# Performance work log

Measured on AMD Instinct MI355X. Metric: run time of the kernel, lower is better.

## Reference

```python
import jax, jax.numpy as jnp
import numpy as np

V, D, E, K = 8192, 128, 262144, 512

def _sqrtm_psd(A):
    # symmetric PSD matrix square root via eigendecomposition
    w, v = jnp.linalg.eigh(A)
    w = jnp.clip(w, 0.0)
    return (v * jnp.sqrt(w)) @ v.T


def setup_inputs() -> dict:
    key = jax.random.key(0)
    k1, k2, k3, k4 = jax.random.split(key, 4)
    inputs = jax.random.normal(k1, (V, D), dtype=jnp.float32) * 0.1
    # targets must be SPD (it is passed through sqrtm as a covariance)
    A = jax.random.normal(k2, (K, K), dtype=jnp.float32) / np.sqrt(K)
    targets = A @ A.T + 0.1 * jnp.eye(K, dtype=jnp.float32)
    edge_index = jax.random.randint(k3, (2, E), 0, V, dtype=jnp.int32)
    pmat = jax.random.normal(k4, (K, V), dtype=jnp.float32) / np.sqrt(V)
    return {"inputs": inputs, "targets": targets, "edge_index": edge_index, "pmat": pmat}


def reference(inputs, targets, edge_index, pmat):
    n = inputs.shape[0]
    i, j = edge_index[0], edge_index[1]
    # per-edge squared distance -> exp weight (vectorized gather-compute)
    d = jnp.sum((inputs[i] - inputs[j]) ** 2, axis=-1)  # [E]
    w = jnp.exp(-d)
    # W starts as identity (self loops give exp(0)=1, same as eye); symmetric scatter
    W = jnp.eye(n, dtype=inputs.dtype)
    W = W.at[i, j].set(w).at[j, i].set(w)
    deg = W.sum(axis=1)
    L = jnp.diag(deg) - W
    k = pmat.shape[0]
    L_adj = pmat @ L @ pmat.T + 1e-05 * jnp.eye(k, dtype=inputs.dtype)
    S1 = jnp.linalg.inv(L_adj)
    S0 = targets.astype(jnp.float32)
    S0_sqrt = _sqrtm_psd(S0)
    S_ = _sqrtm_psd(S0_sqrt @ S1 @ S0_sqrt)
    return jnp.trace(S1) + jnp.trace(S0) - 2.0 * jnp.trace(S_)
```

## Files before the change

### kernel.cpp

```cpp
#include <hip/hip_runtime.h>
#include <math.h>

#define VN 8192
#define DN 128
#define EN 262144
#define KD 512
#define KK (KD*KD)

#define S_SS_LADJ 0
#define S_INV_C1  1
#define S_SS_S0   2
#define S_INV_C0  3
#define S_QRT_C0  4
#define S_SS_G    5
#define S_INV_CG  6
#define S_QRT_CG  7
#define S_TR_X    8
#define S_TR_S0   9
#define S_TR_YG   10

typedef __attribute__((ext_vector_type(8))) __bf16 bf16x8;
typedef __attribute__((ext_vector_type(4))) float f32x4;

static __device__ __forceinline__ float waveReduceAdd(float v) {
#pragma unroll
  for (int o = 32; o; o >>= 1) v += __shfl_xor(v, o);
  return v;
}

static __device__ __forceinline__ ushort f2b(float f) {
  unsigned x = __float_as_uint(f);
  unsigned r = (x + 0x7fffu + ((x >> 16) & 1u)) >> 16;
  return (ushort)r;
}
static __device__ __forceinline__ float b2f(ushort u) {
  return __uint_as_float((unsigned)u << 16);
}


__global__ __launch_bounds__(256) void transpose_k(const float* __restrict__ in,
                                                   float* __restrict__ out) {
  __shared__ float s[32][33];
  int tx = threadIdx.x & 31, ty = threadIdx.x >> 5;
  int v0 = blockIdx.x * 32, k0 = blockIdx.y * 32;
  for (int r = ty; r < 32; r += 8) s[r][tx] = in[(size_t)(k0 + r) * VN + v0 + tx];
  __syncthreads();
  for (int r = ty; r < 32; r += 8) out[(size_t)(v0 + r) * KD + k0 + tx] = s[tx][r];
}

__global__ __launch_bounds__(256) void count_k(const float* __restrict__ x,
                                               const int* __restrict__ ei,
                                               int* __restrict__ ea, int* __restrict__ eb,
                                               float* __restrict__ ew,
                                               int* __restrict__ cnt,
                                               unsigned int* __restrict__ bitmap) {
  int e = (int)(((unsigned)blockIdx.x * 256u + threadIdx.x) >> 4);
  int lane = threadIdx.x & 63;
  int sl = lane & 15;
  if (e >= EN) return;
  int i = ei[e], j = ei[EN + e];
  int a = i < j ? i : j;
  int b = i < j ? j : i;
  int ok = 0;
  if (sl == 0) {
    if (i != j) {
      unsigned key = (unsigned)a * (unsigned)VN + (unsigned)b;
      unsigned m = 1u << (key & 31u);
      unsigned old = atomicOr(bitmap + (key >> 5), m);
      ok = (old & m) ? 0 : 1;
    }
  }
  ok = __shfl(ok, lane & 48);
  if (!ok) { if (sl == 0) ea[e] = -1; return; }
  const float4* xa = (const float4*)&x[(size_t)a * DN + sl * 8];
  const float4* xb = (const float4*)&x[(size_t)b * DN + sl * 8];
  float4 a0 = xa[0], a1 = xa[1], b0 = xb[0], b1 = xb[1];
  float d0 = a0.x - b0.x, d1 = a0.y - b0.y, d2 = a0.z - b0.z, d3 = a0.w - b0.w;
  float d4 = a1.x - b1.x, d5 = a1.y - b1.y, d6 = a1.z - b1.z, d7 = a1.w - b1.w;
  float s = d0*d0 + d1*d1 + d2*d2 + d3*d3 + d4*d4 + d5*d5 + d6*d6 + d7*d7;
#pragma unroll
  for (int o = 8; o; o >>= 1) s += __shfl_xor(s, o);
  if (sl == 0) {
    ea[e] = a; eb[e] = b; ew[e] = expf(-s);
    atomicAdd(cnt + a, 1);
    atomicAdd(cnt + b, 1);
  }
}

__global__ __launch_bounds__(1024) void scan_k(const int* __restrict__ cnt,
                                               int* __restrict__ rowptr,
                                               int* __restrict__ cursor) {
  __shared__ int sd[1024];
  __shared__ int carry;
  int tid = threadIdx.x;
  if (tid == 0) { carry = 0; rowptr[0] = 0; }
  __syncthreads();
  for (int c = 0; c < VN / 1024; ++c) {
    int v = c * 1024 + tid;
    int xv = cnt[v];
    sd[tid] = xv;
    __syncthreads();
    for (int off = 1; off < 1024; off <<= 1) {
      int t = (tid >= off) ? sd[tid - off] : 0;
      __syncthreads();
      sd[tid] += t;
      __syncthreads();
    }
    int incl = sd[tid];
    int base = carry;
    rowptr[v + 1] = base + incl;
    cursor[v] = base + incl - xv;
    __syncthreads();
    if (tid == 1023) carry = base + incl;
    __syncthreads();
  }
}

__global__ __launch_bounds__(256) void fill_k(const int* __restrict__ ea, const int* __restrict__ eb,
                                              const float* __restrict__ ew,
                                              int* __restrict__ cursor,
                                              int* __restrict__ adjj, float* __restrict__ adjw) {
  int e = blockIdx.x * 256 + threadIdx.x;
  if (e >= EN) return;
  int a = ea[e];
  if (a < 0) return;
  int b = eb[e];
  float w = ew[e];
  int p = atomicAdd(cursor + a, 1); adjj[p] = b; adjw[p] = w;
  int q = atomicAdd(cursor + b, 1); adjj[q] = a; adjw[q] = w;
}

__global__ __launch_bounds__(512) void buildB_k(const float* __restrict__ pmatT,
                                                const int* __restrict__ rowptr,
                                                const int* __restrict__ adjj,
                                                const float* __restrict__ adjw,
                                                float* __restrict__ Bout) {
  int v = blockIdx.x;
  int k = threadIdx.x;
  int s = rowptr[v], e = rowptr[v + 1];
  float a0 = 0.f, a1 = 0.f, a2 = 0.f, a3 = 0.f;
  float a4 = 0.f, a5 = 0.f, a6 = 0.f, a7 = 0.f, sw = 0.f;
  int p = s;
  for (; p + 8 <= e; p += 8) {
    int j0 = adjj[p],     j1 = adjj[p + 1], j2 = adjj[p + 2], j3 = adjj[p + 3];
    int j4 = adjj[p + 4], j5 = adjj[p + 5], j6 = adjj[p + 6], j7 = adjj[p + 7];
    float w0 = adjw[p],     w1 = adjw[p + 1], w2 = adjw[p + 2], w3 = adjw[p + 3];
    float w4 = adjw[p + 4], w5 = adjw[p + 5], w6 = adjw[p + 6], w7 = adjw[p + 7];
    a0 += w0 * pmatT[(size_t)j0 * KD + k];
    a1 += w1 * pmatT[(size_t)j1 * KD + k];
    a2 += w2 * pmatT[(size_t)j2 * KD + k];
    a3 += w3 * pmatT[(size_t)j3 * KD + k];
    a4 += w4 * pmatT[(size_t)j4 * KD + k];
    a5 += w5 * pmatT[(size_t)j5 * KD + k];
    a6 += w6 * pmatT[(size_t)j6 * KD + k];
    a7 += w7 * pmatT[(size_t)j7 * KD + k];
    sw += w0 + w1 + w2 + w3 + w4 + w5 + w6 + w7;
  }
  for (; p < e; ++p) {
    int jj = adjj[p];
    float w = adjw[p];
    a0 += w * pmatT[(size_t)jj * KD + k];
    sw += w;
  }
  Bout[(size_t)v * KD + k] = sw * pmatT[(size_t)v * KD + k]
                           - ((a0 + a1) + (a2 + a3) + (a4 + a5) + (a6 + a7));
}

__global__ __launch_bounds__(256) void gemm_big_k(const float* __restrict__ A,
                                                  const float* __restrict__ B,
                                                  float* __restrict__ C) {
  __shared__ __align__(16) float As[32][68];
  __shared__ __align__(16) float Bs[32][68];
  int tid = threadIdx.x;
  int tx = tid & 15, ty = tid >> 4;
  int n0 = blockIdx.x * 64, m0 = blockIdx.y * 64;
  int kbase = blockIdx.z * (VN / 8);
  float acc[4][4] = {};
  for (int kt = kbase; kt < kbase + VN / 8; kt += 32) {
#pragma unroll
    for (int u = 0; u < 2; ++u) {
      int li = tid * 2 + u;
      int r = li >> 3, c = (li & 7) * 4;
      float4 av = *(const float4*)&A[(size_t)(m0 + r) * VN + kt + c];
      As[c][r] = av.x; As[c + 1][r] = av.y; As[c + 2][r] = av.z; As[c + 3][r] = av.w;
      int rb = li >> 4, cb = (li & 15) * 4;
      *(float4*)&Bs[rb][cb] = *(const float4*)&B[(size_t)(kt + rb) * KD + n0 + cb];
    }
    __syncthreads();
#pragma unroll
    for (int k = 0; k < 32; ++k) {
      float4 av = *(const float4*)&As[k][ty * 4];
      float4 bv = *(const float4*)&Bs[k][tx * 4];
      float am[4] = {av.x, av.y, av.z, av.w};
      float bm[4] = {bv.x, bv.y, bv.z, bv.w};
#pragma unroll
      for (int mi = 0; mi < 4; ++mi)
#pragma unroll
        for (int ni = 0; ni < 4; ++ni) acc[mi][ni] += am[mi] * bm[ni];
    }
    __syncthreads();
  }
#pragma unroll
  for (int mi = 0; mi < 4; ++mi)
#pragma unroll
    for (int ni = 0; ni < 4; ++ni)
      atomicAdd(&C[(m0 + ty * 4 + mi) * KD + n0 + tx * 4 + ni], acc[mi][ni]);
}


static __device__ __forceinline__ void g32_body(const float* __restrict__ A,
                                                const float* __restrict__ B,
                                                const float* __restrict__ Dm,
                                                float* __restrict__ C,
                                                float alpha, float beta) {
  __shared__ __align__(16) float As[32][34];
  __shared__ __align__(16) float Bs[32][34];
  int tid = threadIdx.x;
  int tx = tid & 15, ty = tid >> 4;
  int n0 = blockIdx.x * 32, m0 = blockIdx.y * 32;
  float a00 = 0.f, a01 = 0.f, a10 = 0.f, a11 = 0.f;
  for (int kt = 0; kt < KD; kt += 32) {
#pragma unroll
    for (int u = 0; u < 4; ++u) {
      int li = tid * 4 + u;
      int r = li >> 5, c = li & 31;
      As[c][r] = A[(m0 + r) * KD + kt + c];
      Bs[r][c] = B[(kt + r) * KD + n0 + c];
    }
    __syncthreads();
#pragma unroll
    for (int k = 0; k < 32; ++k) {
      float2 av = *(const float2*)&As[k][2 * ty];
      float2 bv = *(const float2*)&Bs[k][2 * tx];
      a00 += av.x * bv.x; a01 += av.x * bv.y;
      a10 += av.y * bv.x; a11 += av.y * bv.y;
    }
    __syncthreads();
  }
  int m = m0 + 2 * ty, n = n0 + 2 * tx;
  float d00 = 0.f, d01 = 0.f, d10 = 0.f, d11 = 0.f;
  if (beta != 0.0f) {
    d00 = Dm[m * KD + n];       d01 = Dm[m * KD + n + 1];
    d10 = Dm[(m + 1) * KD + n]; d11 = Dm[(m + 1) * KD + n + 1];
  }
  C[m * KD + n]           = alpha * a00 + beta * d00;
  C[m * KD + n + 1]       = alpha * a01 + beta * d01;
  C[(m + 1) * KD + n]     = alpha * a10 + beta * d10;
  C[(m + 1) * KD + n + 1] = alpha * a11 + beta * d11;
}

__global__ __launch_bounds__(256) void gemm_kk(const float* __restrict__ A,
                                               const float* __restrict__ B,
                                               const float* __restrict__ Dm,
                                               float* __restrict__ C,
                                               float alpha, float beta) {
  g32_body(A, B, Dm, C, alpha, beta);
}

__global__ __launch_bounds__(256) void gemm_dual32(const float* A0, const float* B0,
                                                   const float* D0, float* C0,
                                                   float alpha0, float beta0,
                                                   const float* A1, const float* B1,
                                                   const float* D1, float* C1,
                                                   float alpha1, float beta1) {
  if (blockIdx.z == 0) g32_body(A0, B0, D0, C0, alpha0, beta0);
  else                 g32_body(A1, B1, D1, C1, alpha1, beta1);
}


struct SmemT { ushort a[2][2][64][40]; ushort b[2][2][64][40]; };

static __device__ __forceinline__ void mgemm_s(SmemT* sm,
    const float* Asl, const float* Bsl, const float* Dsl, float* Csl,
    float alpha, float beta, int wsplit) {
  const ushort* Ah = (const ushort*)(Asl + KK);
  const ushort* Al = Ah + KK;
  const ushort* Bh = (const ushort*)(Bsl + KK);
  const ushort* Bl = Bh + KK;
  int tid = threadIdx.x;
  int lane = tid & 63, wave = tid >> 6;
  int wr = wave >> 1, wc = wave & 1;
  int fr = lane & 15, fq = lane >> 4;
  int m0 = blockIdx.y * 64, n0 = blockIdx.x * 64;
  int sr = tid >> 2, skc = (tid & 3) * 8;
  const size_t aoff = (size_t)(m0 + sr) * KD + skc;
  const size_t boff = (size_t)(n0 + sr) * KD + skc;
  f32x4 acc[2][2] = {};
  uint4 va0 = *(const uint4*)&Ah[aoff];
  uint4 va1 = *(const uint4*)&Al[aoff];
  uint4 vb0 = *(const uint4*)&Bh[boff];
  uint4 vb1 = *(const uint4*)&Bl[boff];
  *(uint4*)&sm->a[0][0][sr][skc] = va0;
  *(uint4*)&sm->a[0][1][sr][skc] = va1;
  *(uint4*)&sm->b[0][0][sr][skc] = vb0;
  *(uint4*)&sm->b[0][1][sr][skc] = vb1;
  __syncthreads();
  for (int it = 0; it < 16; ++it) {
    int cur = it & 1, nxt = cur ^ 1;
    if (it < 15) {
      size_t ktn = (size_t)(it + 1) * 32;
      va0 = *(const uint4*)&Ah[aoff + ktn];
      va1 = *(const uint4*)&Al[aoff + ktn];
      vb0 = *(const uint4*)&Bh[boff + ktn];
      vb1 = *(const uint4*)&Bl[boff + ktn];
    }
    bf16x8 ah[2], al[2], bh[2], bl[2];
#pragma unroll
    for (int m = 0; m < 2; ++m) {
      ah[m] = *(const bf16x8*)&sm->a[cur][0][wr * 32 + m * 16 + fr][fq * 8];
      al[m] = *(const bf16x8*)&sm->a[cur][1][wr * 32 + m * 16 + fr][fq * 8];
    }
#pragma unroll
    for (int n = 0; n < 2; ++n) {
      bh[n] = *(const bf16x8*)&sm->b[cur][0][wc * 32 + n * 16 + fr][fq * 8];
      bl[n] = *(const bf16x8*)&sm->b[cur][1][wc * 32 + n * 16 + fr][fq * 8];
    }
#pragma unroll
    for (int m = 0; m < 2; ++m)
#pragma unroll
      for (int n = 0; n < 2; ++n) {
        acc[m][n] = __builtin_amdgcn_mfma_f32_16x16x32_bf16(ah[m], bh[n], acc[m][n], 0, 0, 0);
        acc[m][n] = __builtin_amdgcn_mfma_f32_16x16x32_bf16(ah[m], bl[n], acc[m][n], 0, 0, 0);
        acc[m][n] = __builtin_amdgcn_mfma_f32_16x16x32_bf16(al[m], bh[n], acc[m][n], 0, 0, 0);
      }
    if (it < 15) {
      *(uint4*)&sm->a[nxt][0][sr][skc] = va0;
      *(uint4*)&sm->a[nxt][1][sr][skc] = va1;
      *(uint4*)&sm->b[nxt][0][sr][skc] = vb0;
      *(uint4*)&sm->b[nxt][1][sr][skc] = vb1;
    }
    __syncthreads();
  }
  ushort* Ch = (ushort*)(Csl + KK);
  ushort* Cl = Ch + KK;
#pragma unroll
  for (int m = 0; m < 2; ++m)
#pragma unroll
    for (int n = 0; n < 2; ++n) {
      int col = n0 + wc * 32 + n * 16 + fr;
#pragma unroll
      for (int j = 0; j < 4; ++j) {
        int row = m0 + wr * 32 + m * 16 + fq * 4 + j;
        float v = alpha * acc[m][n][j];
        if (beta != 0.f) v += beta * Dsl[row * KD + col];
        Csl[row * KD + col] = v;
        if (wsplit) {
          ushort h = f2b(v);
          Ch[row * KD + col] = h;
          Cl[row * KD + col] = f2b(v - b2f(h));
        }
      }
    }
}

__global__ __launch_bounds__(256) void bc3_k(const float* Za, const float* Ya, float* Pm,
                                             const float* Xa, const float* Ra,
                                             float* Xb, float* Rb) {
  __shared__ SmemT sm;
  int z = blockIdx.z;
  if (z == 0)      mgemm_s(&sm, Za, Ya, nullptr, Pm, 1.f, 0.f, 1);
  else if (z == 1) mgemm_s(&sm, Xa, Ra, Xa, Xb, 1.f, 1.f, 1);
  else             mgemm_s(&sm, Ra, Ra, nullptr, Rb, 1.f, 0.f, 1);
}

__global__ __launch_bounds__(256) void inv2_k(const float* Xa, const float* Ra,
                                              float* Xb, float* Rb) {
  __shared__ SmemT sm;
  if (blockIdx.z == 0) mgemm_s(&sm, Xa, Ra, Xa, Xb, 1.f, 1.f, 1);
  else                 mgemm_s(&sm, Ra, Ra, nullptr, Rb, 1.f, 0.f, 1);
}

__global__ __launch_bounds__(256) void yz2_k(const float* Ya, const float* Za, const float* Pm,
                                             float* Yb, float* Zb) {
  __shared__ SmemT sm;
  if (blockIdx.z == 0) mgemm_s(&sm, Ya, Pm, Ya, Yb, -0.5f, 1.5f, 1);
  else                 mgemm_s(&sm, Pm, Za, Za, Zb, -0.5f, 1.5f, 1);
}

__global__ __launch_bounds__(256) void pm1_k(const float* Za, const float* Ya, float* Pm) {
  __shared__ SmemT sm;
  mgemm_s(&sm, Za, Ya, nullptr, Pm, 1.f, 0.f, 1);
}


__global__ __launch_bounds__(256) void sumsq_k(const float* __restrict__ A, int n,
                                               float* __restrict__ slot) {
  float s = 0.f;
  for (int i = blockIdx.x * 256 + threadIdx.x; i < n; i += gridDim.x * 256) {
    float v = A[i];
    s += v * v;
  }
  __shared__ float p[4];
  s = waveReduceAdd(s);
  if ((threadIdx.x & 63) == 0) p[threadIdx.x >> 6] = s;
  __syncthreads();
  if (threadIdx.x == 0) atomicAdd(slot, p[0] + p[1] + p[2] + p[3]);
}

__global__ __launch_bounds__(256) void sumsq2_k(const float* __restrict__ A0, float* s0,
                                                const float* __restrict__ A1, float* s1) {
  const float* A = blockIdx.z ? A1 : A0;
  float* slot = blockIdx.z ? s1 : s0;
  float s = 0.f;
  for (int i = blockIdx.x * 256 + threadIdx.x; i < KK; i += gridDim.x * 256) {
    float v = A[i];
    s += v * v;
  }
  __shared__ float p[4];
  s = waveReduceAdd(s);
  if ((threadIdx.x & 63) == 0) p[threadIdx.x >> 6] = s;
  __syncthreads();
  if (threadIdx.x == 0) atomicAdd(slot, p[0] + p[1] + p[2] + p[3]);
}

__global__ __launch_bounds__(512) void trace_k(const float* __restrict__ A,
                                               float* __restrict__ slot) {
  float v = A[(size_t)threadIdx.x * KD + threadIdx.x];
  __shared__ float p[8];
  v = waveReduceAdd(v);
  if ((threadIdx.x & 63) == 0) p[threadIdx.x >> 6] = v;
  __syncthreads();
  if (threadIdx.x == 0) {
    float t = 0.f;
    for (int i = 0; i < 8; ++i) t += p[i];
    slot[0] = t;
  }
}

__global__ __launch_bounds__(512) void trace2_k(const float* __restrict__ A0, float* s0,
                                                const float* __restrict__ A1, float* s1) {
  const float* A = blockIdx.z ? A1 : A0;
  float* slot = blockIdx.z ? s1 : s0;
  float v = A[(size_t)threadIdx.x * KD + threadIdx.x];
  __shared__ float p[8];
  v = waveReduceAdd(v);
  if ((threadIdx.x & 63) == 0) p[threadIdx.x >> 6] = v;
  __syncthreads();
  if (threadIdx.x == 0) {
    float t = 0.f;
    for (int i = 0; i < 8; ++i) t += p[i];
    slot[0] = t;
  }
}

__global__ void derive_k(const float* __restrict__ in, float* __restrict__ o_rsqrt,
                         float* __restrict__ o_qroot) {
  float x = in[0];
  o_rsqrt[0] = 1.0f / sqrtf(x);
  if (o_qroot) o_qroot[0] = powf(x, 0.25f);
}

__global__ void derive2_k(float* __restrict__ scal) {
  if (threadIdx.x == 0) {
    scal[S_INV_C1] = 1.0f / sqrtf(scal[S_SS_LADJ]);
  } else if (threadIdx.x == 1) {
    float x = scal[S_SS_S0];
    scal[S_INV_C0] = 1.0f / sqrtf(x);
    scal[S_QRT_C0] = powf(x, 0.25f);
  }
}

__global__ __launch_bounds__(256) void setid_const_k(float* __restrict__ C, float val) {
  int idx = blockIdx.x * 256 + threadIdx.x;
  int r = idx >> 9, c = idx & (KD - 1);
  C[idx] = (r == c) ? val : 0.0f;
}

__global__ __launch_bounds__(256) void initinv_split_k(const float* __restrict__ Ladj,
                                                       const float* __restrict__ s,
                                                       float* __restrict__ X,
                                                       float* __restrict__ R) {
  int idx = blockIdx.x * 256 + threadIdx.x;
  int r = idx >> 9, c = idx & (KD - 1);
  float cv = s[0];
  float id = (r == c) ? 1.f : 0.f;
  float xv = id * cv;
  float rv = id - cv * Ladj[idx];
  ushort* Xh = (ushort*)(X + KK); ushort* Xl = Xh + KK;
  ushort* Rh = (ushort*)(R + KK); ushort* Rl = Rh + KK;
  X[idx] = xv; ushort h = f2b(xv); Xh[idx] = h; Xl[idx] = f2b(xv - b2f(h));
  R[idx] = rv; h = f2b(rv);        Rh[idx] = h; Rl[idx] = f2b(rv - b2f(h));
}

__global__ __launch_bounds__(256) void prep2_k(const float* __restrict__ A,
                                               const float* __restrict__ s,
                                               float* __restrict__ Cs,
                                               float* __restrict__ Ci) {
  int idx = blockIdx.x * 256 + threadIdx.x;
  if (blockIdx.z == 0) {
    float v = A[idx] * s[0];
    ushort* Chh = (ushort*)(Cs + KK); ushort* Cll = Chh + KK;
    Cs[idx] = v; ushort h = f2b(v); Chh[idx] = h; Cll[idx] = f2b(v - b2f(h));
  } else {
    int r = idx >> 9, c = idx & (KD - 1);
    float v = (r == c) ? 1.0f : 0.0f;
    ushort* Chh = (ushort*)(Ci + KK); ushort* Cll = Chh + KK;
    Ci[idx] = v; ushort h = f2b(v); Chh[idx] = h; Cll[idx] = f2b(v - b2f(h));
  }
}

__global__ __launch_bounds__(256) void scale32_k(const float* __restrict__ A,
                                                 const float* __restrict__ s,
                                                 float* __restrict__ C) {
  int idx = blockIdx.x * 256 + threadIdx.x;
  C[idx] = A[idx] * s[0];
}

__global__ __launch_bounds__(256) void symss_k(const float* __restrict__ G,
                                               float* __restrict__ Out,
                                               float* __restrict__ slot) {
  int idx = blockIdx.x * 256 + threadIdx.x;
  int r = idx >> 9, c = idx & (KD - 1);
  float v = 0.5f * (G[idx] + G[c * KD + r]);
  Out[idx] = v;
  float s = v * v;
  __shared__ float p[4];
  s = waveReduceAdd(s);
  if ((threadIdx.x & 63) == 0) p[threadIdx.x >> 6] = s;
  __syncthreads();
  if (threadIdx.x == 0) atomicAdd(slot, p[0] + p[1] + p[2] + p[3]);
}

__global__ void final_k(const float* __restrict__ scal, float* __restrict__ out) {
  out[0] = scal[S_TR_X] + scal[S_TR_S0] - 2.0f * scal[S_QRT_CG] * scal[S_TR_YG];
}


extern "C" void kernel_launch(void* const* d_in, const int* in_sizes, int n_in,
                              void* d_out, int out_size, void* d_ws, size_t ws_size,
                              hipStream_t stream) {
  (void)in_sizes; (void)n_in; (void)out_size; (void)ws_size;
  const float* x    = (const float*)d_in[0];
  const float* S0   = (const float*)d_in[1];
  const int*   ei   = (const int*)d_in[2];
  const float* pmat = (const float*)d_in[3];
  float* out = (float*)d_out;
  char* ws = (char*)d_ws;
  const size_t MB = 1u << 20;
  const size_t SLOT = 2 * MB;

  unsigned* bitmap = (unsigned*)ws;
  float* pmatT = (float*)(ws + 8 * MB);
  float* Bm    = (float*)(ws + 24 * MB);
  float* Ladj  = (float*)(ws + 40 * MB);
  float* Gs    = (float*)(ws + 41 * MB);
  int*   ea     = (int*)(ws + 40 * MB);
  int*   eb     = (int*)(ws + 41 * MB);
  float* ew     = (float*)(ws + 42 * MB);
  int*   adjj   = (int*)(ws + 43 * MB);
  float* adjw   = (float*)(ws + 45 * MB);
  int*   cnt    = (int*)(ws + 47 * MB);
  int*   rowptr = (int*)(ws + 47 * MB + 64 * 1024);
  int*   cursor = (int*)(ws + 47 * MB + 128 * 1024);
  float* scal   = (float*)(ws + 47 * MB + 256 * 1024);
  float* SL[11];
  for (int i = 0; i < 11; ++i) SL[i] = (float*)(ws + (size_t)i * SLOT);
  float *Xa = SL[0], *Ra = SL[1], *Ya = SL[2], *Za = SL[3];
  float *Xb = SL[4], *Rb = SL[5], *Yb = SL[6], *Zb = SL[7];
  float *Pm = SL[8], *S0h = SL[9], *TMP = SL[10];

  hipMemsetAsync(bitmap, 0, (size_t)VN * VN / 8, stream);
  hipMemsetAsync(cnt, 0, (size_t)VN * 4, stream);
  hipMemsetAsync(scal, 0, 64 * 4, stream);

  transpose_k<<<dim3(VN / 32, KD / 32), 256, 0, stream>>>(pmat, pmatT);
  count_k<<<EN / 16, 256, 0, stream>>>(x, ei, ea, eb, ew, cnt, bitmap);
  scan_k<<<1, 1024, 0, stream>>>(cnt, rowptr, cursor);
  fill_k<<<EN / 256, 256, 0, stream>>>(ea, eb, ew, cursor, adjj, adjw);
  buildB_k<<<VN, 512, 0, stream>>>(pmatT, rowptr, adjj, adjw, Bm);
  setid_const_k<<<KK / 256, 256, 0, stream>>>(Ladj, 1e-5f);
  gemm_big_k<<<dim3(8, 8, 8), 256, 0, stream>>>(pmat, Bm, Ladj);

  sumsq2_k<<<dim3(256, 1, 2), 256, 0, stream>>>(Ladj, &scal[S_SS_LADJ], S0, &scal[S_SS_S0]);
  derive2_k<<<1, 2, 0, stream>>>(scal);
  initinv_split_k<<<KK / 256, 256, 0, stream>>>(Ladj, &scal[S_INV_C1], Xa, Ra);
  prep2_k<<<dim3(KK / 256, 1, 2), 256, 0, stream>>>(S0, &scal[S_INV_C0], Ya, Za);

  for (int r = 0; r < 12; ++r) {
    bc3_k<<<dim3(8, 8, 3), 256, 0, stream>>>(Za, Ya, Pm, Xa, Ra, Xb, Rb);
    yz2_k<<<dim3(8, 8, 2), 256, 0, stream>>>(Ya, Za, Pm, Yb, Zb);
    float* t = Xa; Xa = Xb; Xb = t;
    t = Ra; Ra = Rb; Rb = t;
    t = Ya; Ya = Yb; Yb = t;
    t = Za; Za = Zb; Zb = t;
  }
  for (int r = 0; r < 3; ++r) {
    inv2_k<<<dim3(8, 8, 2), 256, 0, stream>>>(Xa, Ra, Xb, Rb);
    float* t = Xa; Xa = Xb; Xb = t;
    t = Ra; Ra = Rb; Rb = t;
  }

  float* U32  = Xb;
  float* Xfin = Rb;
  gemm_dual32<<<dim3(16, 16, 2), 256, 0, stream>>>(Ladj, Xa, nullptr, U32, 1.0f, 0.0f,
                                                   Za, Ya, nullptr, Pm, 1.0f, 0.0f);
  gemm_dual32<<<dim3(16, 16, 2), 256, 0, stream>>>(Xa, U32, Xa, Xfin, -1.0f, 2.0f,
                                                   Ya, Pm, Ya, Yb, -0.5f, 1.5f);
  trace2_k<<<dim3(1, 1, 2), 512, 0, stream>>>(Xfin, &scal[S_TR_X], S0, &scal[S_TR_S0]);
  scale32_k<<<KK / 256, 256, 0, stream>>>(Yb, &scal[S_QRT_C0], S0h);

  gemm_kk<<<dim3(16, 16), 256, 0, stream>>>(S0h, Xfin, nullptr, TMP, 1.0f, 0.0f);
  gemm_kk<<<dim3(16, 16), 256, 0, stream>>>(TMP, S0h, nullptr, Gs, 1.0f, 0.0f);
  symss_k<<<KK / 256, 256, 0, stream>>>(Gs, TMP, &scal[S_SS_G]);
  derive_k<<<1, 1, 0, stream>>>(&scal[S_SS_G], &scal[S_INV_CG], &scal[S_QRT_CG]);
  prep2_k<<<dim3(KK / 256, 1, 2), 256, 0, stream>>>(TMP, &scal[S_INV_CG], Ya, Za);
  for (int r = 0; r < 20; ++r) {
    pm1_k<<<dim3(8, 8, 1), 256, 0, stream>>>(Za, Ya, Pm);
    yz2_k<<<dim3(8, 8, 2), 256, 0, stream>>>(Ya, Za, Pm, Yb, Zb);
    float* t = Ya; Ya = Yb; Yb = t;
    t = Za; Za = Zb; Zb = t;
  }
  gemm_kk<<<dim3(16, 16), 256, 0, stream>>>(Za, Ya, nullptr, Pm, 1.0f, 0.0f);
  gemm_dual32<<<dim3(16, 16, 2), 256, 0, stream>>>(Ya, Pm, Ya, Yb, -0.5f, 1.5f,
                                                   Pm, Za, Za, Zb, -0.5f, 1.5f);
  gemm_kk<<<dim3(16, 16), 256, 0, stream>>>(Zb, Yb, nullptr, Pm, 1.0f, 0.0f);
  gemm_kk<<<dim3(16, 16), 256, 0, stream>>>(Yb, Pm, Yb, S0h, -0.5f, 1.5f);
  trace_k<<<1, 512, 0, stream>>>(S0h, &scal[S_TR_YG]);

  final_k<<<1, 1, 0, stream>>>(scal, out);
}
```

Before: 1.382 ms.

## Split-K the bf16x3 iteration GEMMs and convert fp32 to hi/lo in-kernel

Each 512x512 iteration GEMM is split into two K-halves written to separate partial buffers, which doubles the number of blocks per launch (up to 384). Consumers sum the two partials when they load. The precomputed bf16 hi/lo split copies are removed, and the split is now done on the fly while loading shared memory. Epilogues no longer write split copies. The cost is extra fp32 reads (partials summed, fp32 instead of bf16 pairs) and conversion ALU work in the inner loop, in exchange for better CU occupancy on a small grid and less epilogue traffic.

```diff
diff --git a/kernel.cpp b/kernel.cpp
--- a/kernel.cpp
+++ b/kernel.cpp
@@ -268,41 +268,64 @@
 }
 
 
+struct GDesc {
+  const float *A0, *A1, *B0, *B1, *D0, *D1;
+  float* C;
+  float alpha, beta;
+  int k0, niter;
+};
+struct GPack { GDesc g[6]; };
+
 struct SmemT { ushort a[2][2][64][40]; ushort b[2][2][64][40]; };
 
-static __device__ __forceinline__ void mgemm_s(SmemT* sm,
-    const float* Asl, const float* Bsl, const float* Dsl, float* Csl,
-    float alpha, float beta, int wsplit) {
-  const ushort* Ah = (const ushort*)(Asl + KK);
-  const ushort* Al = Ah + KK;
-  const ushort* Bh = (const ushort*)(Bsl + KK);
-  const ushort* Bl = Bh + KK;
+static __device__ __forceinline__ void load8(float* v, const float* P0,
+                                             const float* P1, size_t off) {
+  float4 x0 = *(const float4*)&P0[off];
+  float4 x1 = *(const float4*)&P0[off + 4];
+  v[0] = x0.x; v[1] = x0.y; v[2] = x0.z; v[3] = x0.w;
+  v[4] = x1.x; v[5] = x1.y; v[6] = x1.z; v[7] = x1.w;
+  if (P1) {
+    float4 y0 = *(const float4*)&P1[off];
+    float4 y1 = *(const float4*)&P1[off + 4];
+    v[0] += y0.x; v[1] += y0.y; v[2] += y0.z; v[3] += y0.w;
+    v[4] += y1.x; v[5] += y1.y; v[6] += y1.z; v[7] += y1.w;
+  }
+}
+
+static __device__ __forceinline__ void cvwrite(SmemT* sm, int buf, int sr, int skc,
+                                               const float* va, const float* vb) {
+  ushort h[8], l[8];
+#pragma unroll
+  for (int i = 0; i < 8; ++i) { h[i] = f2b(va[i]); l[i] = f2b(va[i] - b2f(h[i])); }
+  *(uint4*)&sm->a[buf][0][sr][skc] = *(const uint4*)h;
+  *(uint4*)&sm->a[buf][1][sr][skc] = *(const uint4*)l;
+#pragma unroll
+  for (int i = 0; i < 8; ++i) { h[i] = f2b(vb[i]); l[i] = f2b(vb[i] - b2f(h[i])); }
+  *(uint4*)&sm->b[buf][0][sr][skc] = *(const uint4*)h;
+  *(uint4*)&sm->b[buf][1][sr][skc] = *(const uint4*)l;
+}
+
+static __device__ __forceinline__ void mgemm_s(SmemT* sm, const GDesc& d) {
   int tid = threadIdx.x;
   int lane = tid & 63, wave = tid >> 6;
   int wr = wave >> 1, wc = wave & 1;
   int fr = lane & 15, fq = lane >> 4;
   int m0 = blockIdx.y * 64, n0 = blockIdx.x * 64;
   int sr = tid >> 2, skc = (tid & 3) * 8;
-  const size_t aoff = (size_t)(m0 + sr) * KD + skc;
-  const size_t boff = (size_t)(n0 + sr) * KD + skc;
+  size_t abase = (size_t)(m0 + sr) * KD + d.k0 + skc;
+  size_t bbase = (size_t)(n0 + sr) * KD + d.k0 + skc;
   f32x4 acc[2][2] = {};
-  uint4 va0 = *(const uint4*)&Ah[aoff];
-  uint4 va1 = *(const uint4*)&Al[aoff];
-  uint4 vb0 = *(const uint4*)&Bh[boff];
-  uint4 vb1 = *(const uint4*)&Bl[boff];
-  *(uint4*)&sm->a[0][0][sr][skc] = va0;
-  *(uint4*)&sm->a[0][1][sr][skc] = va1;
-  *(uint4*)&sm->b[0][0][sr][skc] = vb0;
-  *(uint4*)&sm->b[0][1][sr][skc] = vb1;
+  float va[8], vb[8];
+  load8(va, d.A0, d.A1, abase);
+  load8(vb, d.B0, d.B1, bbase);
+  cvwrite(sm, 0, sr, skc, va, vb);
   __syncthreads();
-  for (int it = 0; it < 16; ++it) {
+  for (int it = 0; it < d.niter; ++it) {
     int cur = it & 1, nxt = cur ^ 1;
-    if (it < 15) {
-      size_t ktn = (size_t)(it + 1) * 32;
-      va0 = *(const uint4*)&Ah[aoff + ktn];
-      va1 = *(const uint4*)&Al[aoff + ktn];
-      vb0 = *(const uint4*)&Bh[boff + ktn];
-      vb1 = *(const uint4*)&Bl[boff + ktn];
+    bool more = (it + 1 < d.niter);
+    if (more) {
+      load8(va, d.A0, d.A1, abase + (size_t)(it + 1) * 32);
+      load8(vb, d.B0, d.B1, bbase + (size_t)(it + 1) * 32);
     }
     bf16x8 ah[2], al[2], bh[2], bl[2];
 #pragma unroll
@@ -323,16 +346,9 @@
         acc[m][n] = __builtin_amdgcn_mfma_f32_16x16x32_bf16(ah[m], bl[n], acc[m][n], 0, 0, 0);
         acc[m][n] = __builtin_amdgcn_mfma_f32_16x16x32_bf16(al[m], bh[n], acc[m][n], 0, 0, 0);
       }
-    if (it < 15) {
-      *(uint4*)&sm->a[nxt][0][sr][skc] = va0;
-      *(uint4*)&sm->a[nxt][1][sr][skc] = va1;
-      *(uint4*)&sm->b[nxt][0][sr][skc] = vb0;
-      *(uint4*)&sm->b[nxt][1][sr][skc] = vb1;
-    }
-    __syncthreads();
-  }
-  ushort* Ch = (ushort*)(Csl + KK);
-  ushort* Cl = Ch + KK;
+    if (more) cvwrite(sm, nxt, sr, skc, va, vb);
+    __syncthreads();
+  }
 #pragma unroll
   for (int m = 0; m < 2; ++m)
 #pragma unroll
@@ -341,61 +357,22 @@
 #pragma unroll
       for (int j = 0; j < 4; ++j) {
         int row = m0 + wr * 32 + m * 16 + fq * 4 + j;
-        float v = alpha * acc[m][n][j];
-        if (beta != 0.f) v += beta * Dsl[row * KD + col];
-        Csl[row * KD + col] = v;
-        if (wsplit) {
-          ushort h = f2b(v);
-          Ch[row * KD + col] = h;
-          Cl[row * KD + col] = f2b(v - b2f(h));
+        float v = d.alpha * acc[m][n][j];
+        if (d.beta != 0.f) {
+          float dv = d.D0[row * KD + col];
+          if (d.D1) dv += d.D1[row * KD + col];
+          v += d.beta * dv;
         }
+        d.C[row * KD + col] = v;
       }
     }
 }
 
-__global__ __launch_bounds__(256) void bc3_k(const float* Za, const float* Ya, float* Pm,
-                                             const float* Xa, const float* Ra,
-                                             float* Xb, float* Rb) {
+__global__ __launch_bounds__(256) void mg_k(GPack p) {
   __shared__ SmemT sm;
-  int z = blockIdx.z;
-  if (z == 0)      mgemm_s(&sm, Za, Ya, nullptr, Pm, 1.f, 0.f, 1);
-  else if (z == 1) mgemm_s(&sm, Xa, Ra, Xa, Xb, 1.f, 1.f, 1);
-  else             mgemm_s(&sm, Ra, Ra, nullptr, Rb, 1.f, 0.f, 1);
-}
-
-__global__ __launch_bounds__(256) void inv2_k(const float* Xa, const float* Ra,
-                                              float* Xb, float* Rb) {
-  __shared__ SmemT sm;
-  if (blockIdx.z == 0) mgemm_s(&sm, Xa, Ra, Xa, Xb, 1.f, 1.f, 1);
-  else                 mgemm_s(&sm, Ra, Ra, nullptr, Rb, 1.f, 0.f, 1);
-}
-
-__global__ __launch_bounds__(256) void yz2_k(const float* Ya, const float* Za, const float* Pm,
-                                             float* Yb, float* Zb) {
-  __shared__ SmemT sm;
-  if (blockIdx.z == 0) mgemm_s(&sm, Ya, Pm, Ya, Yb, -0.5f, 1.5f, 1);
-  else                 mgemm_s(&sm, Pm, Za, Za, Zb, -0.5f, 1.5f, 1);
-}
-
-__global__ __launch_bounds__(256) void pm1_k(const float* Za, const float* Ya, float* Pm) {
-  __shared__ SmemT sm;
-  mgemm_s(&sm, Za, Ya, nullptr, Pm, 1.f, 0.f, 1);
-}
-
-
-__global__ __launch_bounds__(256) void sumsq_k(const float* __restrict__ A, int n,
-                                               float* __restrict__ slot) {
-  float s = 0.f;
-  for (int i = blockIdx.x * 256 + threadIdx.x; i < n; i += gridDim.x * 256) {
-    float v = A[i];
-    s += v * v;
-  }
-  __shared__ float p[4];
-  s = waveReduceAdd(s);
-  if ((threadIdx.x & 63) == 0) p[threadIdx.x >> 6] = s;
-  __syncthreads();
-  if (threadIdx.x == 0) atomicAdd(slot, p[0] + p[1] + p[2] + p[3]);
-}
+  mgemm_s(&sm, p.g[blockIdx.z]);
+}
+
 
 __global__ __launch_bounds__(256) void sumsq2_k(const float* __restrict__ A0, float* s0,
                                                 const float* __restrict__ A1, float* s1) {
@@ -466,36 +443,28 @@
   C[idx] = (r == c) ? val : 0.0f;
 }
 
-__global__ __launch_bounds__(256) void initinv_split_k(const float* __restrict__ Ladj,
-                                                       const float* __restrict__ s,
-                                                       float* __restrict__ X,
-                                                       float* __restrict__ R) {
+__global__ __launch_bounds__(256) void initinv32_k(const float* __restrict__ Ladj,
+                                                   const float* __restrict__ s,
+                                                   float* __restrict__ X,
+                                                   float* __restrict__ R) {
   int idx = blockIdx.x * 256 + threadIdx.x;
   int r = idx >> 9, c = idx & (KD - 1);
   float cv = s[0];
   float id = (r == c) ? 1.f : 0.f;
-  float xv = id * cv;
-  float rv = id - cv * Ladj[idx];
-  ushort* Xh = (ushort*)(X + KK); ushort* Xl = Xh + KK;
-  ushort* Rh = (ushort*)(R + KK); ushort* Rl = Rh + KK;
-  X[idx] = xv; ushort h = f2b(xv); Xh[idx] = h; Xl[idx] = f2b(xv - b2f(h));
-  R[idx] = rv; h = f2b(rv);        Rh[idx] = h; Rl[idx] = f2b(rv - b2f(h));
-}
-
-__global__ __launch_bounds__(256) void prep2_k(const float* __restrict__ A,
-                                               const float* __restrict__ s,
-                                               float* __restrict__ Cs,
-                                               float* __restrict__ Ci) {
+  X[idx] = id * cv;
+  R[idx] = id - cv * Ladj[idx];
+}
+
+__global__ __launch_bounds__(256) void prep32_k(const float* __restrict__ A,
+                                                const float* __restrict__ s,
+                                                float* __restrict__ Cs,
+                                                float* __restrict__ Ci) {
   int idx = blockIdx.x * 256 + threadIdx.x;
   if (blockIdx.z == 0) {
-    float v = A[idx] * s[0];
-    ushort* Chh = (ushort*)(Cs + KK); ushort* Cll = Chh + KK;
-    Cs[idx] = v; ushort h = f2b(v); Chh[idx] = h; Cll[idx] = f2b(v - b2f(h));
+    Cs[idx] = A[idx] * s[0];
   } else {
     int r = idx >> 9, c = idx & (KD - 1);
-    float v = (r == c) ? 1.0f : 0.0f;
-    ushort* Chh = (ushort*)(Ci + KK); ushort* Cll = Chh + KK;
-    Ci[idx] = v; ushort h = f2b(v); Chh[idx] = h; Cll[idx] = f2b(v - b2f(h));
+    Ci[idx] = (r == c) ? 1.0f : 0.0f;
   }
 }
 
@@ -523,6 +492,23 @@
 
 __global__ void final_k(const float* __restrict__ scal, float* __restrict__ out) {
   out[0] = scal[S_TR_X] + scal[S_TR_S0] - 2.0f * scal[S_QRT_CG] * scal[S_TR_YG];
+}
+
+
+static inline GDesc mk(const float* A0, const float* A1,
+                       const float* B0, const float* B1,
+                       const float* D0, const float* D1,
+                       float* C, float al, float be, int k0, int ni) {
+  GDesc d;
+  d.A0 = A0; d.A1 = A1; d.B0 = B0; d.B1 = B1; d.D0 = D0; d.D1 = D1;
+  d.C = C; d.alpha = al; d.beta = be; d.k0 = k0; d.niter = ni;
+  return d;
+}
+
+static inline void lp(hipStream_t st, const GDesc* g, int n) {
+  GPack p{};
+  for (int i = 0; i < n; ++i) p.g[i] = g[i];
+  mg_k<<<dim3(8, 8, n), 256, 0, st>>>(p);
 }
 
 
@@ -555,8 +541,8 @@
   float* scal   = (float*)(ws + 47 * MB + 256 * 1024);
   float* SL[11];
   for (int i = 0; i < 11; ++i) SL[i] = (float*)(ws + (size_t)i * SLOT);
-  float *Xa = SL[0], *Ra = SL[1], *Ya = SL[2], *Za = SL[3];
-  float *Xb = SL[4], *Rb = SL[5], *Yb = SL[6], *Zb = SL[7];
+  float *vXa = SL[0], *vRa = SL[1], *vYa = SL[2], *vZa = SL[3];
+  float *vXb = SL[4], *vRb = SL[5], *vYb = SL[6], *vZb = SL[7];
   float *Pm = SL[8], *S0h = SL[9], *TMP = SL[10];
 
   hipMemsetAsync(bitmap, 0, (size_t)VN * VN / 8, stream);
@@ -573,48 +559,99 @@
 
   sumsq2_k<<<dim3(256, 1, 2), 256, 0, stream>>>(Ladj, &scal[S_SS_LADJ], S0, &scal[S_SS_S0]);
   derive2_k<<<1, 2, 0, stream>>>(scal);
-  initinv_split_k<<<KK / 256, 256, 0, stream>>>(Ladj, &scal[S_INV_C1], Xa, Ra);
-  prep2_k<<<dim3(KK / 256, 1, 2), 256, 0, stream>>>(S0, &scal[S_INV_C0], Ya, Za);
+  initinv32_k<<<KK / 256, 256, 0, stream>>>(Ladj, &scal[S_INV_C1], vXa, vRa);
+  prep32_k<<<dim3(KK / 256, 1, 2), 256, 0, stream>>>(S0, &scal[S_INV_C0], vYa, vZa);
+
+  const float *Xa1 = nullptr, *Ra1 = nullptr, *Ya1 = nullptr, *Za1 = nullptr;
 
   for (int r = 0; r < 12; ++r) {
-    bc3_k<<<dim3(8, 8, 3), 256, 0, stream>>>(Za, Ya, Pm, Xa, Ra, Xb, Rb);
-    yz2_k<<<dim3(8, 8, 2), 256, 0, stream>>>(Ya, Za, Pm, Yb, Zb);
-    float* t = Xa; Xa = Xb; Xb = t;
-    t = Ra; Ra = Rb; Rb = t;
-    t = Ya; Ya = Yb; Yb = t;
-    t = Za; Za = Zb; Zb = t;
-  }
-  for (int r = 0; r < 3; ++r) {
-    inv2_k<<<dim3(8, 8, 2), 256, 0, stream>>>(Xa, Ra, Xb, Rb);
-    float* t = Xa; Xa = Xb; Xb = t;
-    t = Ra; Ra = Rb; Rb = t;
-  }
-
-  float* U32  = Xb;
-  float* Xfin = Rb;
-  gemm_dual32<<<dim3(16, 16, 2), 256, 0, stream>>>(Ladj, Xa, nullptr, U32, 1.0f, 0.0f,
-                                                   Za, Ya, nullptr, Pm, 1.0f, 0.0f);
-  gemm_dual32<<<dim3(16, 16, 2), 256, 0, stream>>>(Xa, U32, Xa, Xfin, -1.0f, 2.0f,
-                                                   Ya, Pm, Ya, Yb, -0.5f, 1.5f);
+    bool lastYZ = (r == 11);
+    GDesc g1[6] = {
+      mk(vZa, Za1, vYa, Ya1, nullptr, nullptr, Pm,      1.f, 0.f, 0,   8),
+      mk(vZa, Za1, vYa, Ya1, nullptr, nullptr, Pm + KK, 1.f, 0.f, 256, 8),
+      mk(vXa, Xa1, vRa, Ra1, vXa, Xa1,         vXb,      1.f, 1.f, 0,   8),
+      mk(vXa, Xa1, vRa, Ra1, nullptr, nullptr, vXb + KK, 1.f, 0.f, 256, 8),
+      mk(vRa, Ra1, vRa, Ra1, nullptr, nullptr, vRb,      1.f, 0.f, 0,   8),
+      mk(vRa, Ra1, vRa, Ra1, nullptr, nullptr, vRb + KK, 1.f, 0.f, 256, 8)};
+    lp(stream, g1, 6);
+    if (!lastYZ) {
+      GDesc g2[4] = {
+        mk(vYa, Ya1, Pm, Pm + KK, vYa, Ya1,         vYb,      -0.5f, 1.5f, 0,   8),
+        mk(vYa, Ya1, Pm, Pm + KK, nullptr, nullptr, vYb + KK, -0.5f, 0.f,  256, 8),
+        mk(Pm, Pm + KK, vZa, Za1, vZa, Za1,         vZb,      -0.5f, 1.5f, 0,   8),
+        mk(Pm, Pm + KK, vZa, Za1, nullptr, nullptr, vZb + KK, -0.5f, 0.f,  256, 8)};
+      lp(stream, g2, 4);
+    } else {
+      GDesc g2[2] = {
+        mk(vYa, Ya1, Pm, Pm + KK, vYa, Ya1, vYb, -0.5f, 1.5f, 0, 16),
+        mk(Pm, Pm + KK, vZa, Za1, vZa, Za1, vZb, -0.5f, 1.5f, 0, 16)};
+      lp(stream, g2, 2);
+    }
+    float* t;
+    t = vXa; vXa = vXb; vXb = t; Xa1 = vXa + KK;
+    t = vRa; vRa = vRb; vRb = t; Ra1 = vRa + KK;
+    t = vYa; vYa = vYb; vYb = t; Ya1 = lastYZ ? nullptr : vYa + KK;
+    t = vZa; vZa = vZb; vZb = t; Za1 = lastYZ ? nullptr : vZa + KK;
+  }
+  for (int r = 0; r < 2; ++r) {
+    GDesc g[4] = {
+      mk(vXa, Xa1, vRa, Ra1, vXa, Xa1,         vXb,      1.f, 1.f, 0,   8),
+      mk(vXa, Xa1, vRa, Ra1, nullptr, nullptr, vXb + KK, 1.f, 0.f, 256, 8),
+      mk(vRa, Ra1, vRa, Ra1, nullptr, nullptr, vRb,      1.f, 0.f, 0,   8),
+      mk(vRa, Ra1, vRa, Ra1, nullptr, nullptr, vRb + KK, 1.f, 0.f, 256, 8)};
+    lp(stream, g, 4);
+    float* t = vXa; vXa = vXb; vXb = t; Xa1 = vXa + KK;
+    t = vRa; vRa = vRb; vRb = t; Ra1 = vRa + KK;
+  }
+  {
+    GDesc g[1] = { mk(vXa, Xa1, vRa, Ra1, vXa, Xa1, vXb, 1.f, 1.f, 0, 16) };
+    lp(stream, g, 1);
+    float* t = vXa; vXa = vXb; vXb = t; Xa1 = nullptr;
+  }
+
+  float* U32  = vXb;
+  float* Xfin = vRb;
+  gemm_dual32<<<dim3(16, 16, 2), 256, 0, stream>>>(Ladj, vXa, nullptr, U32, 1.0f, 0.0f,
+                                                   vZa, vYa, nullptr, Pm, 1.0f, 0.0f);
+  gemm_dual32<<<dim3(16, 16, 2), 256, 0, stream>>>(vXa, U32, vXa, Xfin, -1.0f, 2.0f,
+                                                   vYa, Pm, vYa, vYb, -0.5f, 1.5f);
   trace2_k<<<dim3(1, 1, 2), 512, 0, stream>>>(Xfin, &scal[S_TR_X], S0, &scal[S_TR_S0]);
-  scale32_k<<<KK / 256, 256, 0, stream>>>(Yb, &scal[S_QRT_C0], S0h);
+  scale32_k<<<KK / 256, 256, 0, stream>>>(vYb, &scal[S_QRT_C0], S0h);
 
   gemm_kk<<<dim3(16, 16), 256, 0, stream>>>(S0h, Xfin, nullptr, TMP, 1.0f, 0.0f);
   gemm_kk<<<dim3(16, 16), 256, 0, stream>>>(TMP, S0h, nullptr, Gs, 1.0f, 0.0f);
   symss_k<<<KK / 256, 256, 0, stream>>>(Gs, TMP, &scal[S_SS_G]);
   derive_k<<<1, 1, 0, stream>>>(&scal[S_SS_G], &scal[S_INV_CG], &scal[S_QRT_CG]);
-  prep2_k<<<dim3(KK / 256, 1, 2), 256, 0, stream>>>(TMP, &scal[S_INV_CG], Ya, Za);
+  prep32_k<<<dim3(KK / 256, 1, 2), 256, 0, stream>>>(TMP, &scal[S_INV_CG], vYa, vZa);
+  Ya1 = Za1 = nullptr;
   for (int r = 0; r < 20; ++r) {
-    pm1_k<<<dim3(8, 8, 1), 256, 0, stream>>>(Za, Ya, Pm);
-    yz2_k<<<dim3(8, 8, 2), 256, 0, stream>>>(Ya, Za, Pm, Yb, Zb);
-    float* t = Ya; Ya = Yb; Yb = t;
-    t = Za; Za = Zb; Zb = t;
-  }
-  gemm_kk<<<dim3(16, 16), 256, 0, stream>>>(Za, Ya, nullptr, Pm, 1.0f, 0.0f);
-  gemm_dual32<<<dim3(16, 16, 2), 256, 0, stream>>>(Ya, Pm, Ya, Yb, -0.5f, 1.5f,
-                                                   Pm, Za, Za, Zb, -0.5f, 1.5f);
-  gemm_kk<<<dim3(16, 16), 256, 0, stream>>>(Zb, Yb, nullptr, Pm, 1.0f, 0.0f);
-  gemm_kk<<<dim3(16, 16), 256, 0, stream>>>(Yb, Pm, Yb, S0h, -0.5f, 1.5f);
+    bool last = (r == 19);
+    GDesc g1[2] = {
+      mk(vZa, Za1, vYa, Ya1, nullptr, nullptr, Pm,      1.f, 0.f, 0,   8),
+      mk(vZa, Za1, vYa, Ya1, nullptr, nullptr, Pm + KK, 1.f, 0.f, 256, 8)};
+    lp(stream, g1, 2);
+    if (!last) {
+      GDesc g2[4] = {
+        mk(vYa, Ya1, Pm, Pm + KK, vYa, Ya1,         vYb,      -0.5f, 1.5f, 0,   8),
+        mk(vYa, Ya1, Pm, Pm + KK, nullptr, nullptr, vYb + KK, -0.5f, 0.f,  256, 8),
+        mk(Pm, Pm + KK, vZa, Za1, vZa, Za1,         vZb,      -0.5f, 1.5f, 0,   8),
+        mk(Pm, Pm + KK, vZa, Za1, nullptr, nullptr, vZb + KK, -0.5f, 0.f,  256, 8)};
+      lp(stream, g2, 4);
+    } else {
+      GDesc g2[2] = {
+        mk(vYa, Ya1, Pm, Pm + KK, vYa, Ya1, vYb, -0.5f, 1.5f, 0, 16),
+        mk(Pm, Pm + KK, vZa, Za1, vZa, Za1, vZb, -0.5f, 1.5f, 0, 16)};
+      lp(stream, g2, 2);
+    }
+    float* t;
+    t = vYa; vYa = vYb; vYb = t; Ya1 = last ? nullptr : vYa + KK;
+    t = vZa; vZa = vZb; vZb = t; Za1 = last ? nullptr : vZa + KK;
+  }
+  gemm_kk<<<dim3(16, 16), 256, 0, stream>>>(vZa, vYa, nullptr, Pm, 1.0f, 0.0f);
+  gemm_dual32<<<dim3(16, 16, 2), 256, 0, stream>>>(vYa, Pm, vYa, vYb, -0.5f, 1.5f,
+                                                   Pm, vZa, vZa, vZb, -0.5f, 1.5f);
+  gemm_kk<<<dim3(16, 16), 256, 0, stream>>>(vZb, vYb, nullptr, Pm, 1.0f, 0.0f);
+  gemm_kk<<<dim3(16, 16), 256, 0, stream>>>(vYb, Pm, vYb, S0h, -0.5f, 1.5f);
   trace_k<<<1, 512, 0, stream>>>(S0h, &scal[S_TR_YG]);
 
   final_k<<<1, 1, 0, stream>>>(scal, out);
```

Measured after the change: 1.551 ms. +12.2%, slower.
